# Kernel optimization log

Hardware: AMD Instinct MI355X
Metric: run time of the kernel (lower is better)

## Reference

```python
import jax, jax.numpy as jnp
import numpy as np

THRESHOLD_FACTOR = 1.25

def setup_inputs() -> dict:
    key = jax.random.key(0)
    r_embed = jax.random.normal(key, (2, 4096, 2), dtype=jnp.float32)
    return {"r_embed": r_embed}

def reference(r_embed):
    # r_embed: [b, n, 2]
    # diff[b,s,t,i] = -r[b,s,i]*r[b,t,i] + r[b,s,i]   (einsum('bsi,bti->bsti', r, -r) + r.unsqueeze(2))
    diff = -r_embed[:, :, None, :] * r_embed[:, None, :, :] + r_embed[:, :, None, :]  # [b,s,t,2]
    dist_sq = jnp.sum(diff * diff, axis=-1)                                            # [b,s,t]
    phase_diff = jnp.arctan2(diff[..., 1], diff[..., 0])
    forward_bias = 0.5 * (1.0 + jnp.cos(phase_diff)) * jnp.exp(-dist_sq)
    mean_dist = jnp.mean(dist_sq, axis=(-1, -2), keepdims=True)
    n = dist_sq.shape[-1] * dist_sq.shape[-2]
    # torch.std default is unbiased (divide by n-1)
    var = jnp.sum((dist_sq - mean_dist) ** 2, axis=(-1, -2), keepdims=True) / (n - 1)
    std_dist = jnp.maximum(jnp.sqrt(var), 1e-6)
    threshold = mean_dist + THRESHOLD_FACTOR * std_dist
    valid_mask = (dist_sq <= threshold).astype(dist_sq.dtype)
    attention = valid_mask * forward_bias
    row_sums = jnp.sum(attention, axis=-1, keepdims=True)
    attention = attention / (row_sums + 1e-8)
    return attention
```

## Files before the change

### kernel.cpp

```cpp
#include <hip/hip_runtime.h>
#include <math.h>

#define N 4096
#define NB 2
#define THRESHOLD_FACTOR 1.25

typedef float v4f __attribute__((ext_vector_type(4)));

__global__ __launch_bounds__(1024) void stats_kernel(const float* __restrict__ r,
                                                     float* __restrict__ thr) {
    int b = blockIdx.x;
    const float* rb = r + (size_t)b * N * 2;
    int tid = threadIdx.x;

    double s[10];
#pragma unroll
    for (int i = 0; i < 10; ++i) s[i] = 0.0;

#pragma unroll
    for (int it = 0; it < N / 1024; ++it) {
        int idx = it * 1024 + tid;
        float x = rb[idx * 2 + 0];
        float y = rb[idx * 2 + 1];
        double a  = (double)x * (double)x;
        double bb = (double)y * (double)y;
        double ax = 1.0 - (double)x;
        double by = 1.0 - (double)y;
        double A  = ax * ax;
        double Bv = by * by;
        s[0] += a;      s[1] += bb;      s[2] += A;      s[3] += Bv;
        s[4] += a * a;  s[5] += bb * bb; s[6] += a * bb;
        s[7] += A * A;  s[8] += Bv * Bv; s[9] += A * Bv;
    }

#pragma unroll
    for (int q = 0; q < 10; ++q) {
#pragma unroll
        for (int off = 32; off > 0; off >>= 1) s[q] += __shfl_down(s[q], off, 64);
    }

    __shared__ double wsums[16][10];
    __shared__ double tot[10];
    int lane = tid & 63;
    int wid = tid >> 6;
    if (lane == 0) {
#pragma unroll
        for (int q = 0; q < 10; ++q) wsums[wid][q] = s[q];
    }
    __syncthreads();
    if (tid < 10) {
        double acc = 0.0;
#pragma unroll
        for (int w = 0; w < 16; ++w) acc += wsums[w][tid];
        tot[tid] = acc;
    }
    __syncthreads();

    if (tid == 0) {
        double pairs = (double)N * (double)N;
        double sum_d  = tot[0] * tot[2] + tot[1] * tot[3];
        double sum_d2 = tot[4] * tot[7] + tot[5] * tot[8] + 2.0 * tot[6] * tot[9];
        double mean = sum_d / pairs;
        double var = (sum_d2 - sum_d * sum_d / pairs) / (pairs - 1.0);
        double sd = sqrt(var);
        if (sd < 1e-6) sd = 1e-6;
        thr[b] = (float)(mean + THRESHOLD_FACTOR * sd);
    }
}

__global__ __launch_bounds__(256) void attn_kernel(const float* __restrict__ r,
                                                   const float* __restrict__ thr,
                                                   float* __restrict__ out) {
    int row = blockIdx.x;
    int b = row >> 12;
    int s = row & (N - 1);
    const float* rb = r + (size_t)b * N * 2;

    float rsx = rb[s * 2 + 0];
    float rsy = rb[s * 2 + 1];
    float threshold = thr[b];

    int tid = threadIdx.x;

    float4 p[4][2];
#pragma unroll
    for (int g = 0; g < 4; ++g) {
        int t0 = g * 1024 + tid * 4;
        p[g][0] = *(const float4*)(rb + (size_t)t0 * 2);
        p[g][1] = *(const float4*)(rb + (size_t)t0 * 2 + 4);
    }

    float vals[16];
    float sum = 0.0f;
#pragma unroll
    for (int g = 0; g < 4; ++g) {
        float tx[4] = {p[g][0].x, p[g][0].z, p[g][1].x, p[g][1].z};
        float ty[4] = {p[g][0].y, p[g][0].w, p[g][1].y, p[g][1].w};
#pragma unroll
        for (int k = 0; k < 4; ++k) {
            float dx = fmaf(-rsx, tx[k], rsx);
            float dy = fmaf(-rsy, ty[k], rsy);
            float d = fmaf(dx, dx, dy * dy);
            float c = (d > 0.0f) ? (dx * __builtin_amdgcn_rsqf(d)) : 1.0f;
            float h = 0.5f * __expf(-d);
            float fb = fmaf(c, h, h);
            float v = (d <= threshold) ? fb : 0.0f;
            vals[g * 4 + k] = v;
            sum += v;
        }
    }

#pragma unroll
    for (int off = 32; off > 0; off >>= 1) sum += __shfl_down(sum, off, 64);
    __shared__ float wsum[4];
    int lane = tid & 63;
    int wid = tid >> 6;
    if (lane == 0) wsum[wid] = sum;
    __syncthreads();
    float total = wsum[0] + wsum[1] + wsum[2] + wsum[3];
    float inv = __builtin_amdgcn_rcpf(total + 1e-8f);

    v4f* outp = (v4f*)(out + (size_t)row * N);
#pragma unroll
    for (int g = 0; g < 4; ++g) {
        int t0 = g * 1024 + tid * 4;
        v4f v4;
        v4.x = vals[g * 4 + 0] * inv;
        v4.y = vals[g * 4 + 1] * inv;
        v4.z = vals[g * 4 + 2] * inv;
        v4.w = vals[g * 4 + 3] * inv;
        __builtin_nontemporal_store(v4, &outp[t0 >> 2]);
    }
}

extern "C" void kernel_launch(void* const* d_in, const int* in_sizes, int n_in,
                              void* d_out, int out_size, void* d_ws, size_t ws_size,
                              hipStream_t stream) {
    const float* r = (const float*)d_in[0];
    float* out = (float*)d_out;
    float* thr = (float*)d_ws;

    stats_kernel<<<NB, 1024, 0, stream>>>(r, thr);
    attn_kernel<<<NB * N, 256, 0, stream>>>(r, thr, out);
}
```

Baseline: 145.1 us.

## Assign one wavefront per attention row and recompute bias values in the store pass

Each 256-thread block now handles four rows, one per 64-lane wavefront, instead of one row per block. The row sum is reduced with wave shuffles and broadcast with readfirstlane, which removes the shared-memory exchange and __syncthreads. The per-element bias is no longer kept in registers between the sum and the normalisation passes. The second pass reloads the inputs and recomputes the bias, roughly doubling the exp/rsq arithmetic in exchange for fewer live registers and no block-level sync.

```diff
diff --git a/kernel.cpp b/kernel.cpp
--- a/kernel.cpp
+++ b/kernel.cpp
@@ -68,10 +68,23 @@
     }
 }
 
+__device__ __forceinline__ float bias_val(float rsx, float rsy, float threshold,
+                                          float tx, float ty) {
+    float dx = fmaf(-rsx, tx, rsx);
+    float dy = fmaf(-rsy, ty, rsy);
+    float d = fmaf(dx, dx, dy * dy);
+    float c = (d > 0.0f) ? (dx * __builtin_amdgcn_rsqf(d)) : 1.0f;
+    float h = 0.5f * __expf(-d);
+    float fb = fmaf(c, h, h);
+    return (d <= threshold) ? fb : 0.0f;
+}
+
 __global__ __launch_bounds__(256) void attn_kernel(const float* __restrict__ r,
                                                    const float* __restrict__ thr,
                                                    float* __restrict__ out) {
-    int row = blockIdx.x;
+    int lane = threadIdx.x & 63;
+    int wid = threadIdx.x >> 6;
+    int row = blockIdx.x * 4 + wid;
     int b = row >> 12;
     int s = row & (N - 1);
     const float* rb = r + (size_t)b * N * 2;
@@ -80,55 +93,33 @@
     float rsy = rb[s * 2 + 1];
     float threshold = thr[b];
 
-    int tid = threadIdx.x;
-
-    float4 p[4][2];
-#pragma unroll
-    for (int g = 0; g < 4; ++g) {
-        int t0 = g * 1024 + tid * 4;
-        p[g][0] = *(const float4*)(rb + (size_t)t0 * 2);
-        p[g][1] = *(const float4*)(rb + (size_t)t0 * 2 + 4);
-    }
-
-    float vals[16];
     float sum = 0.0f;
 #pragma unroll
-    for (int g = 0; g < 4; ++g) {
-        float tx[4] = {p[g][0].x, p[g][0].z, p[g][1].x, p[g][1].z};
-        float ty[4] = {p[g][0].y, p[g][0].w, p[g][1].y, p[g][1].w};
-#pragma unroll
-        for (int k = 0; k < 4; ++k) {
-            float dx = fmaf(-rsx, tx[k], rsx);
-            float dy = fmaf(-rsy, ty[k], rsy);
-            float d = fmaf(dx, dx, dy * dy);
-            float c = (d > 0.0f) ? (dx * __builtin_amdgcn_rsqf(d)) : 1.0f;
-            float h = 0.5f * __expf(-d);
-            float fb = fmaf(c, h, h);
-            float v = (d <= threshold) ? fb : 0.0f;
-            vals[g * 4 + k] = v;
-            sum += v;
-        }
+    for (int ch = 0; ch < 16; ++ch) {
+        int t0 = ch * 256 + lane * 4;
+        float4 p0 = *(const float4*)(rb + (size_t)t0 * 2);
+        float4 p1 = *(const float4*)(rb + (size_t)t0 * 2 + 4);
+        sum += bias_val(rsx, rsy, threshold, p0.x, p0.y);
+        sum += bias_val(rsx, rsy, threshold, p0.z, p0.w);
+        sum += bias_val(rsx, rsy, threshold, p1.x, p1.y);
+        sum += bias_val(rsx, rsy, threshold, p1.z, p1.w);
     }
-
 #pragma unroll
     for (int off = 32; off > 0; off >>= 1) sum += __shfl_down(sum, off, 64);
-    __shared__ float wsum[4];
-    int lane = tid & 63;
-    int wid = tid >> 6;
-    if (lane == 0) wsum[wid] = sum;
-    __syncthreads();
-    float total = wsum[0] + wsum[1] + wsum[2] + wsum[3];
+    float total = __builtin_amdgcn_readfirstlane(sum);
     float inv = __builtin_amdgcn_rcpf(total + 1e-8f);
 
     v4f* outp = (v4f*)(out + (size_t)row * N);
 #pragma unroll
-    for (int g = 0; g < 4; ++g) {
-        int t0 = g * 1024 + tid * 4;
+    for (int ch = 0; ch < 16; ++ch) {
+        int t0 = ch * 256 + lane * 4;
+        float4 p0 = *(const float4*)(rb + (size_t)t0 * 2);
+        float4 p1 = *(const float4*)(rb + (size_t)t0 * 2 + 4);
         v4f v4;
-        v4.x = vals[g * 4 + 0] * inv;
-        v4.y = vals[g * 4 + 1] * inv;
-        v4.z = vals[g * 4 + 2] * inv;
-        v4.w = vals[g * 4 + 3] * inv;
+        v4.x = bias_val(rsx, rsy, threshold, p0.x, p0.y) * inv;
+        v4.y = bias_val(rsx, rsy, threshold, p0.z, p0.w) * inv;
+        v4.z = bias_val(rsx, rsy, threshold, p1.x, p1.y) * inv;
+        v4.w = bias_val(rsx, rsy, threshold, p1.z, p1.w) * inv;
         __builtin_nontemporal_store(v4, &outp[t0 >> 2]);
     }
 }
@@ -141,5 +132,5 @@
     float* thr = (float*)d_ws;
 
     stats_kernel<<<NB, 1024, 0, stream>>>(r, thr);
-    attn_kernel<<<NB * N, 256, 0, stream>>>(r, thr, out);
+    attn_kernel<<<NB * N / 4, 256, 0, stream>>>(r, thr, out);
 }
```

Result: slower. 155.3 us (+7.0%).

## Fuse threshold statistics into attention kernel, recomputing per row block

Applied to the files above, without the earlier changes.

Removes the separate stats kernel and has every row block recompute the batch-wide moment sums in double precision from the 4096 points it already loads, then derive the threshold locally. This saves one kernel launch and the dependency between the two launches. In exchange, each of the 8192 blocks does redundant FP64 moment accumulation, 10 double shuffle reductions and an extra barrier. The row sum is also switched to double accumulation, which adds more FP64 work.

```diff
diff --git a/kernel.cpp b/kernel.cpp
--- a/kernel.cpp
+++ b/kernel.cpp
@@ -7,80 +7,16 @@
 
 typedef float v4f __attribute__((ext_vector_type(4)));
 
-__global__ __launch_bounds__(1024) void stats_kernel(const float* __restrict__ r,
-                                                     float* __restrict__ thr) {
-    int b = blockIdx.x;
-    const float* rb = r + (size_t)b * N * 2;
-    int tid = threadIdx.x;
-
-    double s[10];
-#pragma unroll
-    for (int i = 0; i < 10; ++i) s[i] = 0.0;
-
-#pragma unroll
-    for (int it = 0; it < N / 1024; ++it) {
-        int idx = it * 1024 + tid;
-        float x = rb[idx * 2 + 0];
-        float y = rb[idx * 2 + 1];
-        double a  = (double)x * (double)x;
-        double bb = (double)y * (double)y;
-        double ax = 1.0 - (double)x;
-        double by = 1.0 - (double)y;
-        double A  = ax * ax;
-        double Bv = by * by;
-        s[0] += a;      s[1] += bb;      s[2] += A;      s[3] += Bv;
-        s[4] += a * a;  s[5] += bb * bb; s[6] += a * bb;
-        s[7] += A * A;  s[8] += Bv * Bv; s[9] += A * Bv;
-    }
-
-#pragma unroll
-    for (int q = 0; q < 10; ++q) {
-#pragma unroll
-        for (int off = 32; off > 0; off >>= 1) s[q] += __shfl_down(s[q], off, 64);
-    }
-
-    __shared__ double wsums[16][10];
-    __shared__ double tot[10];
-    int lane = tid & 63;
-    int wid = tid >> 6;
-    if (lane == 0) {
-#pragma unroll
-        for (int q = 0; q < 10; ++q) wsums[wid][q] = s[q];
-    }
-    __syncthreads();
-    if (tid < 10) {
-        double acc = 0.0;
-#pragma unroll
-        for (int w = 0; w < 16; ++w) acc += wsums[w][tid];
-        tot[tid] = acc;
-    }
-    __syncthreads();
-
-    if (tid == 0) {
-        double pairs = (double)N * (double)N;
-        double sum_d  = tot[0] * tot[2] + tot[1] * tot[3];
-        double sum_d2 = tot[4] * tot[7] + tot[5] * tot[8] + 2.0 * tot[6] * tot[9];
-        double mean = sum_d / pairs;
-        double var = (sum_d2 - sum_d * sum_d / pairs) / (pairs - 1.0);
-        double sd = sqrt(var);
-        if (sd < 1e-6) sd = 1e-6;
-        thr[b] = (float)(mean + THRESHOLD_FACTOR * sd);
-    }
-}
-
-__global__ __launch_bounds__(256) void attn_kernel(const float* __restrict__ r,
-                                                   const float* __restrict__ thr,
-                                                   float* __restrict__ out) {
+__global__ __launch_bounds__(256) void fused_kernel(const float* __restrict__ r,
+                                                    float* __restrict__ out) {
     int row = blockIdx.x;
     int b = row >> 12;
     int s = row & (N - 1);
     const float* rb = r + (size_t)b * N * 2;
 
-    float rsx = rb[s * 2 + 0];
-    float rsy = rb[s * 2 + 1];
-    float threshold = thr[b];
-
     int tid = threadIdx.x;
+    int lane = tid & 63;
+    int wid = tid >> 6;
 
     float4 p[4][2];
 #pragma unroll
@@ -89,9 +25,60 @@
         p[g][0] = *(const float4*)(rb + (size_t)t0 * 2);
         p[g][1] = *(const float4*)(rb + (size_t)t0 * 2 + 4);
     }
+    float rsx = rb[s * 2 + 0];
+    float rsy = rb[s * 2 + 1];
+
+    double st[10];
+#pragma unroll
+    for (int q = 0; q < 10; ++q) st[q] = 0.0;
+
+#pragma unroll
+    for (int g = 0; g < 4; ++g) {
+        float tx[4] = {p[g][0].x, p[g][0].z, p[g][1].x, p[g][1].z};
+        float ty[4] = {p[g][0].y, p[g][0].w, p[g][1].y, p[g][1].w};
+#pragma unroll
+        for (int k = 0; k < 4; ++k) {
+            double x = (double)tx[k];
+            double y = (double)ty[k];
+            double a  = x * x;
+            double bb = y * y;
+            double ax = 1.0 - x;
+            double by = 1.0 - y;
+            double A  = ax * ax;
+            double Bv = by * by;
+            st[0] += a;      st[1] += bb;      st[2] += A;      st[3] += Bv;
+            st[4] += a * a;  st[5] += bb * bb; st[6] += a * bb;
+            st[7] += A * A;  st[8] += Bv * Bv; st[9] += A * Bv;
+        }
+    }
+
+#pragma unroll
+    for (int q = 0; q < 10; ++q) {
+#pragma unroll
+        for (int off = 32; off > 0; off >>= 1) st[q] += __shfl_down(st[q], off, 64);
+    }
+    __shared__ double wsums[4][10];
+    if (lane == 0) {
+#pragma unroll
+        for (int q = 0; q < 10; ++q) wsums[wid][q] = st[q];
+    }
+    __syncthreads();
+
+    double tq[10];
+#pragma unroll
+    for (int q = 0; q < 10; ++q)
+        tq[q] = wsums[0][q] + wsums[1][q] + wsums[2][q] + wsums[3][q];
+    double pairs = (double)N * (double)N;
+    double sum_d  = tq[0] * tq[2] + tq[1] * tq[3];
+    double sum_d2 = tq[4] * tq[7] + tq[5] * tq[8] + 2.0 * tq[6] * tq[9];
+    double mean = sum_d / pairs;
+    double var = (sum_d2 - sum_d * sum_d / pairs) / (pairs - 1.0);
+    double sd = sqrt(var);
+    if (sd < 1e-6) sd = 1e-6;
+    float threshold = (float)(mean + THRESHOLD_FACTOR * sd);
 
     float vals[16];
-    float sum = 0.0f;
+    double dsum = 0.0;
 #pragma unroll
     for (int g = 0; g < 4; ++g) {
         float tx[4] = {p[g][0].x, p[g][0].z, p[g][1].x, p[g][1].z};
@@ -106,19 +93,17 @@
             float fb = fmaf(c, h, h);
             float v = (d <= threshold) ? fb : 0.0f;
             vals[g * 4 + k] = v;
-            sum += v;
+            dsum += (double)v;
         }
     }
 
 #pragma unroll
-    for (int off = 32; off > 0; off >>= 1) sum += __shfl_down(sum, off, 64);
-    __shared__ float wsum[4];
-    int lane = tid & 63;
-    int wid = tid >> 6;
-    if (lane == 0) wsum[wid] = sum;
+    for (int off = 32; off > 0; off >>= 1) dsum += __shfl_down(dsum, off, 64);
+    __shared__ double rsum[4];
+    if (lane == 0) rsum[wid] = dsum;
     __syncthreads();
-    float total = wsum[0] + wsum[1] + wsum[2] + wsum[3];
-    float inv = __builtin_amdgcn_rcpf(total + 1e-8f);
+    double total = rsum[0] + rsum[1] + rsum[2] + rsum[3];
+    float inv = (float)(1.0 / (total + 1e-8));
 
     v4f* outp = (v4f*)(out + (size_t)row * N);
 #pragma unroll
@@ -138,8 +123,7 @@
                               hipStream_t stream) {
     const float* r = (const float*)d_in[0];
     float* out = (float*)d_out;
-    float* thr = (float*)d_ws;
+    (void)d_ws; (void)ws_size;
 
-    stats_kernel<<<NB, 1024, 0, stream>>>(r, thr);
-    attn_kernel<<<NB * N, 256, 0, stream>>>(r, thr, out);
+    fused_kernel<<<NB * N, 256, 0, stream>>>(r, out);
 }
```

After: 173.5 us. +19.5%, slower.
